# Kernel optimization log

Hardware: AMD Instinct MI355X
Metric: run time of the kernel (lower is better)

Reference implementation:

```python
import jax, jax.numpy as jnp
import numpy as np
from functools import partial

ALPHA = 0.5
GAMMA = 0.01
BIG = 1e8  # boundary init, matches compute_softdtw (exp(-BIG/gamma)==0)


def pairwise_sq(x, y):
    # x: [N, d], y: [M, d] -> squared euclidean distances [N, M], clamped at 0
    xn = jnp.sum(x * x, axis=1)[:, None]
    yn = jnp.sum(y * y, axis=1)[None, :]
    d = xn + yn - 2.0 * (x @ y.T)
    return jnp.clip(d, 0.0, None)


def softdtw(D, gamma):
    # soft-DTW DP: V[i,j] = D[i-1,j-1] + softmin(V[i,j-1], V[i-1,j-1], V[i-1,j])
    # scan over rows; inner scan over columns (sequential dependence on V[i,j-1])
    N, M = D.shape

    def row_step(prev_row, d_row):
        # prev_row: V[i-1, 0..M]  (length M+1)
        def col_step(v_left, inp):
            d, v_diag, v_up = inp
            r = jnp.stack([v_left, v_diag, v_up]) * (-1.0 / gamma)
            v = d - gamma * jax.nn.logsumexp(r)  # stable soft-min
            return v, v

        _, row_vals = jax.lax.scan(
            col_step,
            jnp.asarray(BIG, D.dtype),                 # V[i, 0]
            (d_row, prev_row[:-1], prev_row[1:]),      # D[i-1,j-1], V[i-1,j-1], V[i-1,j]
        )
        new_row = jnp.concatenate([jnp.full((1,), BIG, D.dtype), row_vals])
        return new_row, None

    init_row = jnp.concatenate(
        [jnp.zeros((1,), D.dtype), jnp.full((M,), BIG, D.dtype)]
    )  # V[0, :] row with V[0,0]=0
    last_row, _ = jax.lax.scan(row_step, init_row, D)
    return last_row[-1]  # V[N, M]


def dilate_loss(y_pred, y_true, alpha=ALPHA, gamma=GAMMA):
    B, N = y_pred.shape[0], y_pred.shape[1]
    t = y_true.reshape(B, -1, 1)
    o = y_pred.reshape(B, -1, 1)
    D = jax.vmap(pairwise_sq)(t, o)  # [B, N, N]

    sd = partial(softdtw, gamma=gamma)
    # shape term: mean soft-DTW value over batch (SoftDTWBatch)
    loss_shape = jnp.mean(jax.vmap(sd)(D))
    # temporal term: E = d softDTW / d D (soft path), mean over batch (PathDTWBatch)
    path = jnp.mean(jax.vmap(jax.grad(sd))(D), axis=0)  # [N, N]
    idx = jnp.arange(1, N + 1, dtype=y_pred.dtype)
    omega = (idx[:, None] - idx[None, :]) ** 2  # pairwise_distances(range(1,N+1))
    loss_temporal = jnp.sum(path * omega) / (N * N)

    return alpha * loss_shape + (1.0 - alpha) * loss_temporal


def setup_inputs() -> dict:
    key = jax.random.key(0)
    k1, k2 = jax.random.split(key)
    B, N = 64, 256
    y_pred = jax.random.normal(k1, (B, N, 1), dtype=jnp.float32)
    y_true = jax.random.normal(k2, (B, N, 1), dtype=jnp.float32)
    return {"y_pred": y_pred, "y_true": y_true}


def reference(y_pred, y_true):
    return dilate_loss(y_pred, y_true)
```

## Files before the change

kernel.cpp:

```cpp
#include <hip/hip_runtime.h>

#define BATCH 64
#define NN 256
#define CSC   144.26950408889634f
#define RCSC  0.0069314718055994531f
#define BIGS  1.4426950408889634e10f


__device__ __forceinline__ float shr1(float x, float old) {
    return __int_as_float(__builtin_amdgcn_update_dpp(
        __float_as_int(old), __float_as_int(x), 0x138, 0xF, 0xF, false));
}

#define ITER(J, OINJ) {                                              \
    float sA = shr1(A, rdcA);                                        \
    float sU = shr1(U, rdcU);                                        \
    oc = shr1(oc, OINJ);                                             \
    rdcA = rdnA; rdcU = rdnU;                                        \
    float2 rr = ringr[((J) + 9) & 15];             \
    rdnA = rr.x; rdnU = rr.y;                                        \
    float m  = fminf(fminf(A, psA), sA);                             \
    float el = __builtin_amdgcn_exp2f(m - A);                        \
    float ed = __builtin_amdgcn_exp2f(m - psA);                      \
    float eu = __builtin_amdgcn_exp2f(m - sA);                       \
    float s  = el + ed + eu;                                         \
    float x  = T - oc;                                               \
    float nv = fmaf(CSC * x, x, m - __builtin_amdgcn_logf(s));       \
    float num = fmaf(el, U, fmaf(ed, psU, eu * sU));                 \
    float nt  = fmaf(num, __builtin_amdgcn_rcpf(s), dr * dr);        \
    if (l63) ringw[(J)] = make_float2(nv, nt);                       \
    psA = sA; psU = sU; A = nv; U = nt; dr -= 1.0f;                  \
}

__global__ __launch_bounds__(256) void dilate_fused(
    const float* __restrict__ y_pred,
    const float* __restrict__ y_true,
    float* __restrict__ out)
{
    const int b   = blockIdx.x;
    const int tid = threadIdx.x;
    const int w   = tid >> 6;
    const int l   = tid & 63;
    const bool l63 = (l == 63);

    __shared__ float  o_lds[1088];
    __shared__ float2 ring[5][16];

    const float4 z4 = make_float4(0.f, 0.f, 0.f, 0.f);
    if (tid < 128) ((float4*)o_lds)[tid] = z4;
    if (tid >= 128 && tid < 208) ((float4*)o_lds)[tid + 64] = z4;
    if (tid < 64) ((float4*)(o_lds + 512))[tid] =
        ((const float4*)(y_pred + b * NN))[tid];
    if (tid < 80) ((float2*)ring)[tid] = make_float2(BIGS, 0.f);

    const float T = y_true[b * NN + tid];
    __syncthreads();

    float A = BIGS, U = 0.f;
    float psA = (tid == 0) ? 0.f : BIGS;
    float psU = 0.f;
    float oc = 0.f;
    float dr = (float)(2 * tid + 8 * w);
    float rdcA = BIGS, rdcU = 0.f, rdnA = BIGS, rdnU = 0.f;

    float2* ringw = ring[w];
    const float2* ringr = ring[(w == 0) ? 4 : (w - 1)];
    const float4* o4 = ((const float4*)o_lds) + (128 - 18 * w);

    float4 fA = o4[0], fB = o4[1], fC = o4[2], fD = o4[3]; o4 += 4;

    #pragma unroll 1
    for (int blk = 0; blk < 33; ++blk) {
        float4 gA = o4[0], gB = o4[1], gC = o4[2], gD = o4[3]; o4 += 4;
        ITER(0,  fA.x) ITER(1,  fA.y) ITER(2,  fA.z) ITER(3,  fA.w)
        __syncthreads();
        ITER(4,  fB.x) ITER(5,  fB.y) ITER(6,  fB.z) ITER(7,  fB.w)
        __syncthreads();
        ITER(8,  fC.x) ITER(9,  fC.y) ITER(10, fC.z) ITER(11, fC.w)
        __syncthreads();
        ITER(12, fD.x) ITER(13, fD.y) ITER(14, fD.z) ITER(15, fD.w)
        __syncthreads();
        fA = gA; fB = gB; fC = gC; fD = gD;
    }
    ITER(0, fA.x) ITER(1, fA.y) ITER(2, fA.z) ITER(3, fA.w)
    ITER(4, fB.x) ITER(5, fB.y) ITER(6, fB.z)

    if (tid == 255) {
        float loss = 0.5f * (A * RCSC) * (1.0f / BATCH)
                   + 0.5f * U * (1.0f / ((float)BATCH * (float)(NN * NN)));
        atomicAdd(out, loss);
    }
}

extern "C" void kernel_launch(void* const* d_in, const int* in_sizes, int n_in,
                              void* d_out, int out_size, void* d_ws, size_t ws_size,
                              hipStream_t stream)
{
    const float* y_pred = (const float*)d_in[0];
    const float* y_true = (const float*)d_in[1];
    hipMemsetAsync(d_out, 0, sizeof(float), stream);
    dilate_fused<<<BATCH, 256, 0, stream>>>(y_pred, y_true, (float*)d_out);
}
```

Before: 99.45 us.

## Deepen inter-wave ring buffer to cut barriers per step in soft-DTW wavefront

Grows the per-wave LDS ring from 16 to 32 entries, so each wave runs further behind its upstream neighbour. This lets the kernel use one raw s_barrier per 8 anti-diagonal steps instead of one __syncthreads per 4. Each wave now reads its y_pred values from its own pre-shifted LDS row, and ring values are prefetched as float4 pairs one group ahead. The wave skew is larger, so the loop grows from 33x16 to 70x8 iterations plus a tail, and the s_barrier in inline asm no longer gets the memory fence that __syncthreads provides.

```diff
diff --git a/kernel.cpp b/kernel.cpp
--- a/kernel.cpp
+++ b/kernel.cpp
@@ -5,6 +5,8 @@
 #define CSC   144.26950408889634f
 #define RCSC  0.0069314718055994531f
 #define BIGS  1.4426950408889634e10f
+#define OROW  576
+#define NGRP  70
 
 
 __device__ __forceinline__ float shr1(float x, float old) {
@@ -12,13 +14,10 @@
         __float_as_int(old), __float_as_int(x), 0x138, 0xF, 0xF, false));
 }
 
-#define ITER(J, OINJ) {                                              \
-    float sA = shr1(A, rdcA);                                        \
-    float sU = shr1(U, rdcU);                                        \
-    oc = shr1(oc, OINJ);                                             \
-    rdcA = rdnA; rdcU = rdnU;                                        \
-    float2 rr = ringr[((J) + 9) & 15];             \
-    rdnA = rr.x; rdnU = rr.y;                                        \
+#define ITER(AX, AY, OINJ) {                                         \
+    float sA = shr1(A, (AX));                                        \
+    float sU = shr1(U, (AY));                                        \
+    oc = shr1(oc, (OINJ));                                           \
     float m  = fminf(fminf(A, psA), sA);                             \
     float el = __builtin_amdgcn_exp2f(m - A);                        \
     float ed = __builtin_amdgcn_exp2f(m - psA);                      \
@@ -28,7 +27,8 @@
     float nv = fmaf(CSC * x, x, m - __builtin_amdgcn_logf(s));       \
     float num = fmaf(el, U, fmaf(ed, psU, eu * sU));                 \
     float nt  = fmaf(num, __builtin_amdgcn_rcpf(s), dr * dr);        \
-    if (l63) ringw[(J)] = make_float2(nv, nt);                       \
+    if (l63) ringw[ws & 31u] = make_float2(nv, nt);                  \
+    ++ws;                                                            \
     psA = sA; psU = sU; A = nv; U = nt; dr -= 1.0f;                  \
 }
 
@@ -43,16 +43,22 @@
     const int l   = tid & 63;
     const bool l63 = (l == 63);
 
-    __shared__ float  o_lds[1088];
-    __shared__ float2 ring[5][16];
+    __shared__ float  oW[4][OROW];
+    __shared__ float2 ring[5][32];
 
-    const float4 z4 = make_float4(0.f, 0.f, 0.f, 0.f);
-    if (tid < 128) ((float4*)o_lds)[tid] = z4;
-    if (tid >= 128 && tid < 208) ((float4*)o_lds)[tid + 64] = z4;
-    if (tid < 64) ((float4*)(o_lds + 512))[tid] =
-        ((const float4*)(y_pred + b * NN))[tid];
-    if (tid < 80) ((float2*)ring)[tid] = make_float2(BIGS, 0.f);
-
+    {
+        float4* p = (float4*)oW;
+        const float4 z4 = make_float4(0.f, 0.f, 0.f, 0.f);
+        p[tid] = z4; p[tid + 256] = z4;
+        if (tid < 64)  p[tid + 512] = z4;
+        if (tid < 160) ((float2*)ring)[tid] = make_float2(BIGS, 0.f);
+    }
+    __syncthreads();
+    {
+        const float4 ov = ((const float4*)(y_pred + b * NN))[l];
+        float* dst = &oW[w][81 * w + 4 * l];
+        dst[0] = ov.x; dst[1] = ov.y; dst[2] = ov.z; dst[3] = ov.w;
+    }
     const float T = y_true[b * NN + tid];
     __syncthreads();
 
@@ -60,30 +66,40 @@
     float psA = (tid == 0) ? 0.f : BIGS;
     float psU = 0.f;
     float oc = 0.f;
-    float dr = (float)(2 * tid + 8 * w);
-    float rdcA = BIGS, rdcU = 0.f, rdnA = BIGS, rdnU = 0.f;
+    float dr = (float)(145 * w + 2 * l);
 
     float2* ringw = ring[w];
-    const float2* ringr = ring[(w == 0) ? 4 : (w - 1)];
-    const float4* o4 = ((const float4*)o_lds) + (128 - 18 * w);
+    const float* ringr = (const float*)((w == 0) ? ring[4] : ring[w - 1]);
+    const float* orow = oW[w];
+    unsigned ws = 0;
 
-    float4 fA = o4[0], fB = o4[1], fC = o4[2], fD = o4[3]; o4 += 4;
+    float4 ua = *(const float4*)(ringr + 14 * 2);
+    float4 ub = *(const float4*)(ringr + 16 * 2);
+    float4 uc = *(const float4*)(ringr + 18 * 2);
+    float4 ud = *(const float4*)(ringr + 20 * 2);
+    float4 coA = *(const float4*)(orow + 0);
+    float4 coB = *(const float4*)(orow + 4);
 
     #pragma unroll 1
-    for (int blk = 0; blk < 33; ++blk) {
-        float4 gA = o4[0], gB = o4[1], gC = o4[2], gD = o4[3]; o4 += 4;
-        ITER(0,  fA.x) ITER(1,  fA.y) ITER(2,  fA.z) ITER(3,  fA.w)
-        __syncthreads();
-        ITER(4,  fB.x) ITER(5,  fB.y) ITER(6,  fB.z) ITER(7,  fB.w)
-        __syncthreads();
-        ITER(8,  fC.x) ITER(9,  fC.y) ITER(10, fC.z) ITER(11, fC.w)
-        __syncthreads();
-        ITER(12, fD.x) ITER(13, fD.y) ITER(14, fD.z) ITER(15, fD.w)
-        __syncthreads();
-        fA = gA; fB = gB; fC = gC; fD = gD;
+    for (int g = 0; g < NGRP; ++g) {
+        const int S = g << 3;
+        const int base = (S + 22) & 31;
+        const float4 na = *(const float4*)(ringr + ((base    ) & 31) * 2);
+        const float4 nb = *(const float4*)(ringr + ((base + 2) & 31) * 2);
+        const float4 nc = *(const float4*)(ringr + ((base + 4) & 31) * 2);
+        const float4 nd = *(const float4*)(ringr + ((base + 6) & 31) * 2);
+        const float4 noA = *(const float4*)(orow + S + 8);
+        const float4 noB = *(const float4*)(orow + S + 12);
+        ITER(ua.x, ua.y, coA.x) ITER(ua.z, ua.w, coA.y)
+        ITER(ub.x, ub.y, coA.z) ITER(ub.z, ub.w, coA.w)
+        ITER(uc.x, uc.y, coB.x) ITER(uc.z, uc.w, coB.y)
+        ITER(ud.x, ud.y, coB.z) ITER(ud.z, ud.w, coB.w)
+        __asm__ volatile("s_barrier" ::: "memory");
+        ua = na; ub = nb; uc = nc; ud = nd;
+        coA = noA; coB = noB;
     }
-    ITER(0, fA.x) ITER(1, fA.y) ITER(2, fA.z) ITER(3, fA.w)
-    ITER(4, fB.x) ITER(5, fB.y) ITER(6, fB.z)
+    ITER(ua.x, ua.y, coA.x)
+    ITER(ua.z, ua.w, coA.y)
 
     if (tid == 255) {
         float loss = 0.5f * (A * RCSC) * (1.0f / BATCH)
```

After: 102.5 us. 1.03x slower.
